# Kernel tuning notes

Measured on AMD Instinct MI355X. Metric: run time of the kernel, lower is better.

Reference implementation:

```python
import jax, jax.numpy as jnp
import numpy as np

# Module config (matches init_kwargs)
IN_CH, K, N_LAYERS, STRIDE = 4, 4, 2, 2
N_QUBITS = 6           # ceil(log2(4*4*4)) = 6
DIM = 2 ** N_QUBITS    # 64 amplitudes
B, H = 128, 128


def setup_inputs() -> dict:
    key = jax.random.key(0)
    k1, k2 = jax.random.split(key)
    x = jax.random.normal(k1, (B, IN_CH, H, H), dtype=jnp.float32)
    weights = jax.random.normal(k2, (N_LAYERS, N_QUBITS, 3), dtype=jnp.float32)
    return {"x": x, "weights": weights}


def _rot(phi, theta, omega):
    # PennyLane Rot(phi, theta, omega) = RZ(omega) RY(theta) RZ(phi)
    c = jnp.cos(theta / 2).astype(jnp.complex64)
    s = jnp.sin(theta / 2).astype(jnp.complex64)
    ep = jnp.exp(-0.5j * (phi + omega).astype(jnp.complex64))
    em = jnp.exp(-0.5j * (phi - omega).astype(jnp.complex64))
    row0 = jnp.stack([ep * c, -jnp.conj(em) * s])
    row1 = jnp.stack([em * s, jnp.conj(ep) * c])
    return jnp.stack([row0, row1])  # (2,2) complex64


def _apply_1q(state, U, w):
    # state: (N, 2,...,2); wire w -> axis 1+w (wire 0 most significant)
    s = jnp.moveaxis(state, 1 + w, -1)
    s = s @ U.T
    return jnp.moveaxis(s, -1, 1 + w)


def _apply_cnot(state, c, t):
    s = jnp.moveaxis(state, (1 + c, 1 + t), (1, 2))
    s = jnp.stack([s[:, 0], s[:, 1, ::-1]], axis=1)
    return jnp.moveaxis(s, (1, 2), (1 + c, 1 + t))


def _circuit(feat, weights):
    # feat: (N, DIM) amplitude-embedded & normalized features
    state = feat.astype(jnp.complex64).reshape((-1,) + (2,) * N_QUBITS)
    ranges = [(l % (N_QUBITS - 1)) + 1 for l in range(N_LAYERS)]
    for _rep in range(N_LAYERS):  # circuit applies the full template n_layers times
        for l in range(N_LAYERS):
            for w in range(N_QUBITS):
                U = _rot(weights[l, w, 0], weights[l, w, 1], weights[l, w, 2])
                state = _apply_1q(state, U, w)
            r = ranges[l]
            for w in range(N_QUBITS):
                state = _apply_cnot(state, w, (w + r) % N_QUBITS)
    probs = state.real ** 2 + state.imag ** 2
    z = []
    for w in range(N_QUBITS):
        p = jnp.moveaxis(probs, 1 + w, 1).reshape(probs.shape[0], 2, -1)
        z.append(p[:, 0].sum(-1) - p[:, 1].sum(-1))  # <Z_w>
    return jnp.stack(z, axis=1)  # (N, n_qubits)


def reference(x, weights):
    Bx, C, Hx, Wx = x.shape
    oh = (Hx - K) // STRIDE + 1
    idx = (jnp.arange(oh) * STRIDE)[:, None] + jnp.arange(K)  # (oh, K)
    p = x[:, :, idx, :]       # (B, C, oh, K, W)
    p = p[..., idx]           # (B, C, oh, K, oh, K)
    p = jnp.transpose(p, (0, 2, 4, 1, 3, 5)).reshape(Bx * oh * oh, C * K * K)
    feat = jnp.pad(p, ((0, 0), (0, DIM - C * K * K)))  # AmplitudeEmbedding pad_with=0
    feat = feat / jnp.linalg.norm(feat, axis=1, keepdims=True)  # normalize=True
    z = _circuit(feat, weights)                        # (B*oh*oh, n_qubits)
    out = z.reshape(Bx, oh, oh, N_QUBITS).transpose(0, 3, 1, 2)
    return out  # (B, n_qubits, oh, oh)
```

## Files before the change

kernel.cpp:

```cpp
#include <hip/hip_runtime.h>

#define NQ   6
#define DIM  64
#define OH   63
#define HH   128
#define CIN  4
#define NB   128
#define PSTR 80

typedef __attribute__((ext_vector_type(8))) short short8;
typedef __attribute__((ext_vector_type(4))) float f32x4;

__device__ __forceinline__ unsigned bf16_rne_u(float f) {
    unsigned u = __builtin_bit_cast(unsigned, f);
    return (u + 0x7fffu + ((u >> 16) & 1u)) >> 16;
}

#if __has_builtin(__builtin_amdgcn_cvt_pk_bf16_f32)
__device__ __forceinline__ unsigned pk_bf16(float a, float b) {
    typedef __attribute__((ext_vector_type(2))) __bf16 bf16x2_t;
    bf16x2_t v = __builtin_amdgcn_cvt_pk_bf16_f32(a, b);
    return __builtin_bit_cast(unsigned, v);
}
#else
__device__ __forceinline__ unsigned pk_bf16(float a, float b) {
    return bf16_rne_u(a) | (bf16_rne_u(b) << 16);
}
#endif

__global__ __launch_bounds__(64) void build_wfrag(const float* __restrict__ wts,
                                                  short* __restrict__ wfrag) {
    const int i   = threadIdx.x;
    const int col = blockIdx.x;

    const int g = (i < 12) ? i : 0;
    const float phi = wts[g * 3 + 0];
    const float th  = wts[g * 3 + 1];
    const float om  = wts[g * 3 + 2];
    const float hc = cosf(0.5f * th);
    const float hs = sinf(0.5f * th);
    const float ap = -0.5f * (phi + om);
    const float am = -0.5f * (phi - om);
    const float ga = cosf(ap) * hc;
    const float gb = sinf(ap) * hc;
    const float gc = cosf(am) * hs;
    const float gd = sinf(am) * hs;

    float2 amp = make_float2(i == col ? 1.0f : 0.0f, 0.0f);

    for (int rep = 0; rep < 2; ++rep) {
        for (int l = 0; l < 2; ++l) {
            for (int w = 0; w < NQ; ++w) {
                const int src = l * 6 + w;
                const float a = __shfl(ga, src, 64);
                const float b = __shfl(gb, src, 64);
                const float c = __shfl(gc, src, 64);
                const float d = __shfl(gd, src, 64);
                const int p = 5 - w;
                const int bbit = (i >> p) & 1;
                const float px = __shfl_xor(amp.x, 1 << p, 64);
                const float py = __shfl_xor(amp.y, 1 << p, 64);
                const float uax = a;
                const float uay = bbit ? -b : b;
                const float ubx = bbit ? c : -c;
                const float uby = d;
                float2 na;
                na.x = uax * amp.x - uay * amp.y + ubx * px - uby * py;
                na.y = uax * amp.y + uay * amp.x + ubx * py + uby * px;
                amp = na;
            }
            const int r = (l == 0) ? 1 : 2;
            for (int w = 0; w < NQ; ++w) {
                const int pc = 5 - w;
                const int pt = 5 - ((w + r) % NQ);
                const int src = i ^ (((i >> pc) & 1) << pt);
                const float nx = __shfl(amp.x, src, 64);
                const float ny = __shfl(amp.y, src, 64);
                amp = make_float2(nx, ny);
            }
        }
    }

    const int t    = col >> 5;
    const int quad = (col >> 3) & 3;
    const int j    = col & 7;
    const int lre  = quad * 16 + (i & 15);
    const int fre  = ((i >> 4)    ) * 2 + t;
    const int fim  = ((i >> 4) + 4) * 2 + t;
    wfrag[(fre * 64 + lre) * 8 + j] = (short)bf16_rne_u(amp.x);
    wfrag[(fim * 64 + lre) * 8 + j] = (short)bf16_rne_u(amp.y);

    {
        const int n  = i & 15;
        const int qq = i >> 4;
#pragma unroll
        for (int tt = 0; tt < 2; ++tt) {
            short8 v;
#pragma unroll
            for (int jj = 0; jj < 8; ++jj) {
                const int k = tt * 32 + qq * 8 + jj;
                unsigned short s;
                if (n < 6)       s = ((k >> (5 - n)) & 1) ? 0xBF80 : 0x3F80;
                else if (n == 6) s = 0x3F80;
                else             s = 0;
                v[jj] = (short)s;
            }
            ((int4*)wfrag)[(16 + tt) * 64 + i] = __builtin_bit_cast(int4, v);
        }
    }
}

__global__ __launch_bounds__(256, 3) void qconv_mfma(const float* __restrict__ x,
                                                     const short* __restrict__ wfrag,
                                                     float* __restrict__ out) {
    __shared__ __align__(16) short sP[4][16 * PSTR];

    const int tid  = threadIdx.x;
    const int lane = tid & 63;
    const int wv   = tid >> 6;
    const int n    = lane & 15;
    const int qq   = lane >> 4;

    const int bid   = blockIdx.x;
    const int row   = (bid >> 1) * 4 + wv;
    const int half2 = (bid & 1) * 2;
    const int b     = row / OH;
    const int oy    = row - b * OH;

    const int c0  = qq >> 1;
    const int kh0 = (qq & 1) * 2;
    const float* xb  = x + (size_t)b * CIN * HH * HH;
    const float* r00 = xb + ((c0    ) * HH + 2 * oy + kh0    ) * HH;
    const float* r01 = xb + ((c0    ) * HH + 2 * oy + kh0 + 1) * HH;
    const float* r10 = xb + ((c0 + 2) * HH + 2 * oy + kh0    ) * HH;
    const float* r11 = xb + ((c0 + 2) * HH + 2 * oy + kh0 + 1) * HH;

#define LOAD8(dst, chg_)                                                     \
    {                                                                        \
        const int oxl_ = min((chg_) * 16 + n, OH - 1);                       \
        const int fo_  = 2 * oxl_;                                           \
        dst[0] = *(const float2*)(r00 + fo_);                                \
        dst[1] = *(const float2*)(r00 + fo_ + 2);                            \
        dst[2] = *(const float2*)(r01 + fo_);                                \
        dst[3] = *(const float2*)(r01 + fo_ + 2);                            \
        dst[4] = *(const float2*)(r10 + fo_);                                \
        dst[5] = *(const float2*)(r10 + fo_ + 2);                            \
        dst[6] = *(const float2*)(r11 + fo_);                                \
        dst[7] = *(const float2*)(r11 + fo_ + 2);                            \
    }

    float2 cur[8];
    LOAD8(cur, half2)

    short8 wfr[8][2], sfr[2];
    {
        const int4* wp = (const int4*)wfrag;
#pragma unroll
        for (int mt = 0; mt < 8; ++mt)
#pragma unroll
            for (int t = 0; t < 2; ++t)
                wfr[mt][t] = __builtin_bit_cast(short8, wp[(mt * 2 + t) * 64 + lane]);
#pragma unroll
        for (int t = 0; t < 2; ++t)
            sfr[t] = __builtin_bit_cast(short8, wp[(16 + t) * 64 + lane]);
    }

    short* myP = sP[wv];

#pragma unroll
    for (int ch = 0; ch < 2; ++ch) {
        float2 nxt[8];
        if (ch < 1) LOAD8(nxt, half2 + 1)

        uint4 u0, u1;
        u0.x = pk_bf16(cur[0].x, cur[0].y);  u0.y = pk_bf16(cur[1].x, cur[1].y);
        u0.z = pk_bf16(cur[2].x, cur[2].y);  u0.w = pk_bf16(cur[3].x, cur[3].y);
        u1.x = pk_bf16(cur[4].x, cur[4].y);  u1.y = pk_bf16(cur[5].x, cur[5].y);
        u1.z = pk_bf16(cur[6].x, cur[6].y);  u1.w = pk_bf16(cur[7].x, cur[7].y);
        const short8 bf0 = __builtin_bit_cast(short8, u0);
        const short8 bf1 = __builtin_bit_cast(short8, u1);

        f32x4 acc[8];
#pragma unroll
        for (int mt = 0; mt < 8; ++mt) acc[mt] = (f32x4){0.f, 0.f, 0.f, 0.f};
#pragma unroll
        for (int mt = 0; mt < 8; ++mt) {
            acc[mt] = __builtin_amdgcn_mfma_f32_16x16x32_bf16(wfr[mt][0], bf0, acc[mt], 0, 0, 0);
            acc[mt] = __builtin_amdgcn_mfma_f32_16x16x32_bf16(wfr[mt][1], bf1, acc[mt], 0, 0, 0);
        }

#pragma unroll
        for (int mt = 0; mt < 4; ++mt) {
            const float p0 = acc[mt][0] * acc[mt][0] + acc[mt + 4][0] * acc[mt + 4][0];
            const float p1 = acc[mt][1] * acc[mt][1] + acc[mt + 4][1] * acc[mt + 4][1];
            const float p2 = acc[mt][2] * acc[mt][2] + acc[mt + 4][2] * acc[mt + 4][2];
            const float p3 = acc[mt][3] * acc[mt][3] + acc[mt + 4][3] * acc[mt + 4][3];
            const unsigned w0 = pk_bf16(p0, p1);
            const unsigned w1 = pk_bf16(p2, p3);
            *((uint2*)(((unsigned*)myP) + n * (PSTR / 2) + mt * 8 + qq * 2)) =
                make_uint2(w0, w1);
        }

        const short8 p0f = *(const short8*)(myP + n * PSTR + qq * 8);
        const short8 p1f = *(const short8*)(myP + n * PSTR + 32 + qq * 8);
        f32x4 c2 = (f32x4){0.f, 0.f, 0.f, 0.f};
        c2 = __builtin_amdgcn_mfma_f32_16x16x32_bf16(sfr[0], p0f, c2, 0, 0, 0);
        c2 = __builtin_amdgcn_mfma_f32_16x16x32_bf16(sfr[1], p1f, c2, 0, 0, 0);

        const float norm = __shfl(c2[2], 16 + n, 64);
        const float inv  = 1.0f / norm;
        const int ox = (half2 + ch) * 16 + n;
        if (ox < OH) {
            float* ob = out + ((size_t)b * NQ * OH + oy) * OH + ox;
            if (qq == 0) {
#pragma unroll
                for (int r = 0; r < 4; ++r)
                    __builtin_nontemporal_store(c2[r] * inv, ob + (size_t)r * (OH * OH));
            } else if (qq == 1) {
                __builtin_nontemporal_store(c2[0] * inv, ob + (size_t)4 * (OH * OH));
                __builtin_nontemporal_store(c2[1] * inv, ob + (size_t)5 * (OH * OH));
            }
        }

        if (ch < 1) {
#pragma unroll
            for (int i = 0; i < 8; ++i) cur[i] = nxt[i];
        }
    }
#undef LOAD8
}

extern "C" void kernel_launch(void* const* d_in, const int* in_sizes, int n_in,
                              void* d_out, int out_size, void* d_ws, size_t ws_size,
                              hipStream_t stream) {
    const float* x   = (const float*)d_in[0];
    const float* wts = (const float*)d_in[1];
    float* out = (float*)d_out;
    short* wfrag = (short*)d_ws;

    build_wfrag<<<64, 64, 0, stream>>>(wts, wfrag);
    qconv_mfma<<<(NB * OH) / 2, 256, 0, stream>>>(x, wfrag, out);
}
```

Measured before the change: 93.89 us.

## Use single-wave blocks with XCD-interleaved work mapping and upfront loads

Blocks shrink from four waves to one, so each block processes one (row, half) unit. Block IDs are remapped so consecutive units land on the same XCD (bid&7 selects a contiguous range of 2016 units), which improves L2 locality between the two halves and neighbouring rows. Both chunks' global loads are now issued at kernel start rather than prefetched in the loop. The cost is four times as many blocks and slightly higher register pressure from holding both load buffers.

```diff
diff --git a/kernel.cpp b/kernel.cpp
--- a/kernel.cpp
+++ b/kernel.cpp
@@ -110,20 +110,19 @@
     }
 }
 
-__global__ __launch_bounds__(256, 3) void qconv_mfma(const float* __restrict__ x,
-                                                     const short* __restrict__ wfrag,
-                                                     float* __restrict__ out) {
-    __shared__ __align__(16) short sP[4][16 * PSTR];
-
-    const int tid  = threadIdx.x;
-    const int lane = tid & 63;
-    const int wv   = tid >> 6;
+__global__ __launch_bounds__(64, 3) void qconv_mfma(const float* __restrict__ x,
+                                                    const short* __restrict__ wfrag,
+                                                    float* __restrict__ out) {
+    __shared__ __align__(16) short sP[16 * PSTR];
+
+    const int lane = threadIdx.x;
     const int n    = lane & 15;
     const int qq   = lane >> 4;
 
     const int bid   = blockIdx.x;
-    const int row   = (bid >> 1) * 4 + wv;
-    const int half2 = (bid & 1) * 2;
+    const int unit  = (bid & 7) * 2016 + (bid >> 3);
+    const int row   = unit >> 1;
+    const int half2 = (unit & 1) * 2;
     const int b     = row / OH;
     const int oy    = row - b * OH;
 
@@ -149,8 +148,9 @@
         dst[7] = *(const float2*)(r11 + fo_ + 2);                            \
     }
 
-    float2 cur[8];
+    float2 cur[8], nxt[8];
     LOAD8(cur, half2)
+    LOAD8(nxt, half2 + 1)
 
     short8 wfr[8][2], sfr[2];
     {
@@ -165,18 +165,15 @@
             sfr[t] = __builtin_bit_cast(short8, wp[(16 + t) * 64 + lane]);
     }
 
-    short* myP = sP[wv];
-
 #pragma unroll
     for (int ch = 0; ch < 2; ++ch) {
-        float2 nxt[8];
-        if (ch < 1) LOAD8(nxt, half2 + 1)
+        const float2* f = (ch == 0) ? cur : nxt;
 
         uint4 u0, u1;
-        u0.x = pk_bf16(cur[0].x, cur[0].y);  u0.y = pk_bf16(cur[1].x, cur[1].y);
-        u0.z = pk_bf16(cur[2].x, cur[2].y);  u0.w = pk_bf16(cur[3].x, cur[3].y);
-        u1.x = pk_bf16(cur[4].x, cur[4].y);  u1.y = pk_bf16(cur[5].x, cur[5].y);
-        u1.z = pk_bf16(cur[6].x, cur[6].y);  u1.w = pk_bf16(cur[7].x, cur[7].y);
+        u0.x = pk_bf16(f[0].x, f[0].y);  u0.y = pk_bf16(f[1].x, f[1].y);
+        u0.z = pk_bf16(f[2].x, f[2].y);  u0.w = pk_bf16(f[3].x, f[3].y);
+        u1.x = pk_bf16(f[4].x, f[4].y);  u1.y = pk_bf16(f[5].x, f[5].y);
+        u1.z = pk_bf16(f[6].x, f[6].y);  u1.w = pk_bf16(f[7].x, f[7].y);
         const short8 bf0 = __builtin_bit_cast(short8, u0);
         const short8 bf1 = __builtin_bit_cast(short8, u1);
 
@@ -197,12 +194,12 @@
             const float p3 = acc[mt][3] * acc[mt][3] + acc[mt + 4][3] * acc[mt + 4][3];
             const unsigned w0 = pk_bf16(p0, p1);
             const unsigned w1 = pk_bf16(p2, p3);
-            *((uint2*)(((unsigned*)myP) + n * (PSTR / 2) + mt * 8 + qq * 2)) =
+            *((uint2*)(((unsigned*)sP) + n * (PSTR / 2) + mt * 8 + qq * 2)) =
                 make_uint2(w0, w1);
         }
 
-        const short8 p0f = *(const short8*)(myP + n * PSTR + qq * 8);
-        const short8 p1f = *(const short8*)(myP + n * PSTR + 32 + qq * 8);
+        const short8 p0f = *(const short8*)(sP + n * PSTR + qq * 8);
+        const short8 p1f = *(const short8*)(sP + n * PSTR + 32 + qq * 8);
         f32x4 c2 = (f32x4){0.f, 0.f, 0.f, 0.f};
         c2 = __builtin_amdgcn_mfma_f32_16x16x32_bf16(sfr[0], p0f, c2, 0, 0, 0);
         c2 = __builtin_amdgcn_mfma_f32_16x16x32_bf16(sfr[1], p1f, c2, 0, 0, 0);
@@ -220,11 +217,6 @@
                 __builtin_nontemporal_store(c2[0] * inv, ob + (size_t)4 * (OH * OH));
                 __builtin_nontemporal_store(c2[1] * inv, ob + (size_t)5 * (OH * OH));
             }
-        }
-
-        if (ch < 1) {
-#pragma unroll
-            for (int i = 0; i < 8; ++i) cur[i] = nxt[i];
         }
     }
 #undef LOAD8
@@ -239,5 +231,5 @@
     short* wfrag = (short*)d_ws;
 
     build_wfrag<<<64, 64, 0, stream>>>(wts, wfrag);
-    qconv_mfma<<<(NB * OH) / 2, 256, 0, stream>>>(x, wfrag, out);
-}
+    qconv_mfma<<<NB * OH * 2, 64, 0, stream>>>(x, wfrag, out);
+}
```

Result: no change. 95.73 us (+2.0%).
